# Kernel tuning notes

Hardware: AMD Instinct MI355X
Metric: run time of the kernel (lower is better)

Reference implementation:

```python
import jax, jax.numpy as jnp
import numpy as np

# Dimensions: B jets, P max particles, C coords, F features, K neighbors,
# H hidden units, O MLP output dim. Edge feature dim E = 2*(C+F).
B, P, C, F, K, H, O = 256, 128, 2, 7, 16, 128, 256
E = 2 * (C + F)
BIG = 1e9  # distance assigned to invalid (padded) neighbors


def setup_inputs() -> dict:
    key = jax.random.key(0)
    k1, k2, k3, k4 = jax.random.split(key, 4)
    raw = jax.random.normal(k1, (B, P, C + F), dtype=jnp.float32)
    # per-jet particle counts in [K+2, P]; padding is contiguous at the end
    lengths = jax.random.randint(k2, (B,), K + 2, P + 1)
    mask = (jnp.arange(P)[None, :] < lengths[:, None]).astype(jnp.float32)  # [B,P]
    # zero out padded rows and append mask as the last column (as the layer expects)
    x = jnp.concatenate([raw * mask[..., None], mask[..., None]], axis=-1)  # [B,P,C+F+1]
    W1 = jax.random.normal(k3, (E, H), dtype=jnp.float32) * (1.0 / np.sqrt(E))
    b1 = jnp.zeros((H,), dtype=jnp.float32)
    W2 = jax.random.normal(k4, (H, O), dtype=jnp.float32) * (1.0 / np.sqrt(H))
    b2 = jnp.zeros((O,), dtype=jnp.float32)
    return {"x": x, "W1": W1, "b1": b1, "W2": W2, "b2": b2}


def reference(x, W1, b1, W2, b2):
    coords = x[..., :C]          # [B,P,C]
    feats = x[..., C:-1]         # [B,P,F]
    mask = x[..., -1]            # [B,P] 1=real particle, 0=padding
    valid = mask > 0

    # --- kNN on coordinates (masked, vectorized over jets) ---
    diff = coords[:, :, None, :] - coords[:, None, :, :]      # [B,P,P,C]
    # squared distance: same ordering as tf.norm, avoids sqrt-at-zero issues
    dist2 = jnp.sum(diff * diff, axis=-1)                      # [B,P,P]
    dist2 = jnp.where(valid[:, None, :], dist2, BIG)           # mask padded neighbors
    _, idx = jax.lax.top_k(-dist2, K + 1)                      # [B,P,K+1]
    idx = idx[..., 1:]                                         # drop self -> [B,P,K]

    # --- gather neighbor coords/features ---
    idx_flat = idx.reshape(B, P * K)
    nbr_c = jnp.take_along_axis(coords, idx_flat[..., None], axis=1).reshape(B, P, K, C)
    nbr_f = jnp.take_along_axis(feats, idx_flat[..., None], axis=1).reshape(B, P, K, F)
    ctr_c = jnp.broadcast_to(coords[:, :, None, :], (B, P, K, C))
    ctr_f = jnp.broadcast_to(feats[:, :, None, :], (B, P, K, F))

    # edge features: [coord_i, feat_i, coord_j - coord_i, feat_j - feat_i]
    edge = jnp.concatenate([ctr_c, ctr_f, nbr_c - ctr_c, nbr_f - ctr_f], axis=-1)  # [B,P,K,E]

    # --- MLP + mean aggregation over neighbors ---
    h = jax.nn.relu(edge @ W1 + b1)   # [B,P,K,H]
    h = jax.nn.relu(h @ W2 + b2)      # [B,P,K,O]
    avg = jnp.mean(h, axis=2)         # [B,P,O]

    # append mask column; zero out padded particles (matches _fix_number_of_particles)
    out = jnp.concatenate([avg, jnp.ones((B, P, 1), avg.dtype)], axis=-1) * mask[..., None]
    return out
```

## Files before the change

kernel.cpp:

```cpp
#include <hip/hip_runtime.h>

#define BB 256
#define PP 128
#define KK 16
#define HH 128
#define OO 256
#define EE 18
#define XCH 10
#define BIGD 1000000000.0f
#define GPT 4

typedef __bf16 bf16x8 __attribute__((ext_vector_type(8)));
typedef __bf16 bf16x4 __attribute__((ext_vector_type(4)));
typedef float  f32x4  __attribute__((ext_vector_type(4)));

__global__ __launch_bounds__(256) void pack_w_kernel(const float* __restrict__ W1,
                                                     const float* __restrict__ W2,
                                                     __bf16* __restrict__ W2p,
                                                     __bf16* __restrict__ W1p) {
    const int t = blockIdx.x * 256 + threadIdx.x;
    if (t < 32768) {
        const int j  = t & 7;
        const int l  = (t >> 3) & 63;
        const int ks = (t >> 9) & 3;
        const int ct = t >> 11;
        const int row = ks * 32 + ((l >> 4) * 8) + j;
        const int col = ct * 16 + (l & 15);
        W2p[t] = (__bf16)W2[row * OO + col];
    } else {
        const int t2 = t - 32768;
        const int j  = t2 & 7;
        const int l  = (t2 >> 3) & 63;
        const int nt = t2 >> 9;
        const int k  = ((l >> 4) * 8) + j;
        const int n  = nt * 16 + (l & 15);
        W1p[t2] = (k < EE) ? (__bf16)W1[k * HH + n] : (__bf16)0.0f;
    }
}

__global__ __launch_bounds__(256, 4) void mlp_kernel(const float* __restrict__ x,
                                                     const __bf16* __restrict__ W1p,
                                                     const float* __restrict__ b1,
                                                     const __bf16* __restrict__ W2p,
                                                     const float* __restrict__ b2,
                                                     float* __restrict__ out) {
    __shared__ __bf16 sh1A[16 * 64 * 8];
    __shared__ float  sb1[HH];
    __shared__ float  sb2[OO];
    __shared__ float  smask[GPT];
    __shared__ int    sknn[GPT][KK];

    const int tid = threadIdx.x;
    const int lane = tid & 63;
    const int w = tid >> 6;
    const int quad = lane >> 4;
    const int lcol = lane & 15;

    const int pbase = blockIdx.x * GPT;
    const int bidx = pbase >> 7;
    const int i0 = pbase & (PP - 1);
    const float* xb = x + (size_t)bidx * PP * XCH;
    float* outrow = out + (size_t)pbase * (OO + 1);

    if (tid < HH) sb1[tid] = b1[tid];
    sb2[tid] = b2[tid];
    if (tid < GPT) smask[tid] = xb[(i0 + tid) * XCH + (XCH - 1)];
    __syncthreads();

    const bool allmasked =
        (smask[0] == 0.0f) & (smask[1] == 0.0f) & (smask[2] == 0.0f) & (smask[3] == 0.0f);
    if (allmasked) {
        for (int o = tid; o < GPT * (OO + 1); o += 256) outrow[o] = 0.0f;
        return;
    }

    const int i = i0 + w;
    if (smask[w] != 0.0f) {
        const float cix = xb[i * XCH + 0];
        const float ciy = xb[i * XCH + 1];

        const int j0 = lane, j1 = lane + 64;
        float d0, d1;
        {
            const float2 c0 = *(const float2*)(xb + j0 * XCH);
            const float m0 = xb[j0 * XCH + (XCH - 1)];
            float dx = cix - c0.x, dy = ciy - c0.y;
            d0 = __fadd_rn(__fmul_rn(dx, dx), __fmul_rn(dy, dy));
            if (m0 <= 0.0f || j0 == i) d0 = BIGD;
        }
        {
            const float2 c1 = *(const float2*)(xb + j1 * XCH);
            const float m1 = xb[j1 * XCH + (XCH - 1)];
            float dx = cix - c1.x, dy = ciy - c1.y;
            d1 = __fadd_rn(__fmul_rn(dx, dx), __fmul_rn(dy, dy));
            if (m1 <= 0.0f || j1 == i) d1 = BIGD;
        }

        const unsigned d0b = __float_as_uint(d0);
        const unsigned d1b = __float_as_uint(d1);

        unsigned long long A0 = ~0ull, A1 = ~0ull, W0 = 0ull, W1 = 0ull;
        int need = KK;
        int asz = 2 * 64;

        auto step = [&](unsigned long long q0, unsigned long long q1) {
            const unsigned long long z0 = A0 & q0;
            const unsigned long long z1 = A1 & q1;
            const int c = __popcll(z0) + __popcll(z1);
            if (c == need) { W0 |= z0; W1 |= z1; A0 = A1 = 0ull; need = 0; }
            else if (c > need) { A0 = z0; A1 = z1; asz = c; }
            else { W0 |= z0; W1 |= z1; need -= c; A0 &= ~z0; A1 &= ~z1; asz -= c; }
        };

#pragma unroll 1
        for (int t = 14; t >= 0; --t) {
            const unsigned dg0 = (d0b >> (2 * t + 1)) & 3u;
            const unsigned dg1 = (d1b >> (2 * t + 1)) & 3u;
            const unsigned long long p0_0  = __ballot(dg0 == 0u);
            const unsigned long long p1_0  = __ballot(dg1 == 0u);
            const unsigned long long p0_01 = __ballot(dg0 <= 1u);
            const unsigned long long p1_01 = __ballot(dg1 <= 1u);
            const unsigned long long p0_02 = __ballot(dg0 <= 2u);
            const unsigned long long p1_02 = __ballot(dg1 <= 2u);
            const unsigned long long z0_0  = A0 & p0_0,  z1_0  = A1 & p1_0;
            const unsigned long long z0_01 = A0 & p0_01, z1_01 = A1 & p1_01;
            const unsigned long long z0_02 = A0 & p0_02, z1_02 = A1 & p1_02;
            const int c0  = __popcll(z0_0)  + __popcll(z1_0);
            const int c01 = __popcll(z0_01) + __popcll(z1_01);
            const int c02 = __popcll(z0_02) + __popcll(z1_02);
            if (c0 >= need) {
                A0 = z0_0; A1 = z1_0; asz = c0;
            } else if (c01 >= need) {
                W0 |= z0_0; W1 |= z1_0; need -= c0;
                A0 = z0_01 & ~p0_0; A1 = z1_01 & ~p1_0; asz = c01 - c0;
            } else if (c02 >= need) {
                W0 |= z0_01; W1 |= z1_01; need -= c01;
                A0 = z0_02 & ~p0_01; A1 = z1_02 & ~p1_01; asz = c02 - c01;
            } else {
                W0 |= z0_02; W1 |= z1_02; need -= c02;
                A0 &= ~p0_02; A1 &= ~p1_02; asz -= c02;
            }
            if (asz == need) { W0 |= A0; W1 |= A1; A0 = A1 = 0ull; need = 0; break; }
        }
        if (need) {
            const unsigned long long q0 = __ballot((d0b & 1u) == 0u);
            const unsigned long long q1 = __ballot((d1b & 1u) == 0u);
            step(q0, q1);
        }
        if (need) step(~0ull, 0ull);
        {
            const unsigned long long M5 = 0x00000000FFFFFFFFull;
            const unsigned long long M4 = 0x0000FFFF0000FFFFull;
            const unsigned long long M3 = 0x00FF00FF00FF00FFull;
            const unsigned long long M2 = 0x0F0F0F0F0F0F0F0Full;
            const unsigned long long M1 = 0x3333333333333333ull;
            const unsigned long long M0 = 0x5555555555555555ull;
            if (need) step(M5, M5);
            if (need) step(M4, M4);
            if (need) step(M3, M3);
            if (need) step(M2, M2);
            if (need) step(M1, M1);
            if (need) step(M0, M0);
        }
        W0 |= A0; W1 |= A1;

        unsigned int mb0 = __builtin_amdgcn_mbcnt_lo((unsigned)(W0 & 0xffffffffull), 0u);
        mb0 = __builtin_amdgcn_mbcnt_hi((unsigned)(W0 >> 32), mb0);
        unsigned int mb1 = __builtin_amdgcn_mbcnt_lo((unsigned)(W1 & 0xffffffffull), 0u);
        mb1 = __builtin_amdgcn_mbcnt_hi((unsigned)(W1 >> 32), mb1);
        const int base1 = __popcll(W0);

        if ((W0 >> lane) & 1ull) sknn[w][mb0] = j0;
        if ((W1 >> lane) & 1ull) sknn[w][base1 + mb1] = j1;
    } else {
        if (lane < KK) sknn[w][lane] = 0;
    }

    const int jn = sknn[w][lcol];
    const float* ci = xb + i * XCH;
    const float* cj = xb + jn * XCH;
    const float2 a01 = *(const float2*)(ci + 0);
    const float2 a23 = *(const float2*)(ci + 2);
    const float2 a45 = *(const float2*)(ci + 4);
    const float2 a67 = *(const float2*)(ci + 6);
    const float  a8  = ci[8];
    const float2 n01 = *(const float2*)(cj + 0);
    const float2 n23 = *(const float2*)(cj + 2);
    const float2 n45 = *(const float2*)(cj + 4);
    const float2 n67 = *(const float2*)(cj + 6);
    const float  n8  = cj[8];

    float v[8];
#pragma unroll
    for (int e = 0; e < 8; ++e) v[e] = 0.0f;
    if (quad == 0) {
        v[0] = a01.x; v[1] = a01.y; v[2] = a23.x; v[3] = a23.y;
        v[4] = a45.x; v[5] = a45.y; v[6] = a67.x; v[7] = a67.y;
    } else if (quad == 1) {
        v[0] = a8;
        v[1] = n01.x - a01.x; v[2] = n01.y - a01.y;
        v[3] = n23.x - a23.x; v[4] = n23.y - a23.y;
        v[5] = n45.x - a45.x; v[6] = n45.y - a45.y;
        v[7] = n67.x - a67.x;
    } else if (quad == 2) {
        v[0] = n67.y - a67.y;
        v[1] = n8 - a8;
    }

    bf16x8 ef;
#pragma unroll
    for (int e = 0; e < 8; ++e) ef[e] = (__bf16)v[e];

    bf16x8 wf[8];
#pragma unroll
    for (int nt = 0; nt < 8; ++nt)
        wf[nt] = *(const bf16x8*)&W1p[(size_t)((nt * 64 + lane) * 8)];

    const f32x4 z4 = {0.0f, 0.0f, 0.0f, 0.0f};
    f32x4 h[8];
#pragma unroll
    for (int nt = 0; nt < 8; ++nt)
        h[nt] = __builtin_amdgcn_mfma_f32_16x16x32_bf16(wf[nt], ef, z4, 0, 0, 0);

#pragma unroll
    for (int nt = 0; nt < 8; ++nt) {
        const int ks = nt >> 1;
        const int lp = (((nt * 2 + (quad >> 1)) & 3) << 4) | lcol;
        bf16x4 hv;
#pragma unroll
        for (int r = 0; r < 4; ++r) {
            const int m = nt * 16 + quad * 4 + r;
            hv[r] = (__bf16)fmaxf(h[nt][r] + sb1[m], 0.0f);
        }
        *(bf16x4*)&sh1A[((ks * GPT + w) * 64 + lp) * 8 + (quad & 1) * 4] = hv;
    }
    __syncthreads();

    f32x4 acc[GPT][4];
#pragma unroll
    for (int g = 0; g < GPT; ++g)
#pragma unroll
        for (int ct = 0; ct < 4; ++ct) acc[g][ct] = z4;

#pragma unroll
    for (int ks = 0; ks < 4; ++ks) {
        bf16x8 af[GPT], bfr[4];
#pragma unroll
        for (int g = 0; g < GPT; ++g)
            af[g] = *(const bf16x8*)&sh1A[((ks * GPT + g) * 64 + lane) * 8];
#pragma unroll
        for (int ct = 0; ct < 4; ++ct)
            bfr[ct] = *(const bf16x8*)&W2p[(size_t)((((w * 4 + ct) * 4 + ks) * 64 + lane) * 8)];
#pragma unroll
        for (int g = 0; g < GPT; ++g)
#pragma unroll
            for (int ct = 0; ct < 4; ++ct)
                acc[g][ct] = __builtin_amdgcn_mfma_f32_16x16x32_bf16(
                    af[g], bfr[ct], acc[g][ct], 0, 0, 0);
    }

    float val[4];
#pragma unroll
    for (int g = 0; g < GPT; ++g) {
#pragma unroll
        for (int ct = 0; ct < 4; ++ct) {
            const int col = w * 64 + ct * 16 + lcol;
            const float bc = sb2[col];
            float s = 0.0f;
#pragma unroll
            for (int r = 0; r < 4; ++r) s += fmaxf(acc[g][ct][r] + bc, 0.0f);
            s += __shfl_xor(s, 16, 64);
            s += __shfl_xor(s, 32, 64);
            if (quad == g) val[ct] = s;
        }
    }
    const float m = smask[quad] * (1.0f / KK);
#pragma unroll
    for (int ct = 0; ct < 4; ++ct)
        outrow[(size_t)quad * (OO + 1) + w * 64 + ct * 16 + lcol] = val[ct] * m;
    if (tid < GPT) outrow[(size_t)tid * (OO + 1) + OO] = smask[tid];
}

extern "C" void kernel_launch(void* const* d_in, const int* in_sizes, int n_in,
                              void* d_out, int out_size, void* d_ws, size_t ws_size,
                              hipStream_t stream) {
    const float* x  = (const float*)d_in[0];
    const float* W1 = (const float*)d_in[1];
    const float* b1 = (const float*)d_in[2];
    const float* W2 = (const float*)d_in[3];
    const float* b2 = (const float*)d_in[4];
    float* out = (float*)d_out;

    __bf16* W2p = (__bf16*)d_ws;
    __bf16* W1p = (__bf16*)((char*)d_ws + 65536);

    pack_w_kernel<<<144, 256, 0, stream>>>(W1, W2, W2p, W1p);

    const int nblocks = (BB * PP) / GPT;
    mlp_kernel<<<nblocks, 256, 0, stream>>>(x, W1p, b1, W2p, b2, out);
}
```

Measured before the change: 128.7 us.

## Convert MLP kernel to persistent grid-stride loop over particle chunks

The kernel now launches a fixed grid of 2048 blocks. Each block loops over several 4-particle chunks instead of launching one block per chunk, so the per-block bias loading and launch overhead are paid once per block rather than once per chunk. The mask values are read into registers directly rather than staged through shared memory. An extra barrier per iteration is added to protect the shared h1 buffer from being overwritten before the previous chunk's readers finish. This costs some latency hiding, because fewer independent blocks are in flight.

```diff
diff --git a/kernel.cpp b/kernel.cpp
--- a/kernel.cpp
+++ b/kernel.cpp
@@ -9,6 +9,7 @@
 #define XCH 10
 #define BIGD 1000000000.0f
 #define GPT 4
+#define NBLK 2048
 
 typedef __bf16 bf16x8 __attribute__((ext_vector_type(8)));
 typedef __bf16 bf16x4 __attribute__((ext_vector_type(4)));
@@ -47,7 +48,6 @@
     __shared__ __bf16 sh1A[16 * 64 * 8];
     __shared__ float  sb1[HH];
     __shared__ float  sb2[OO];
-    __shared__ float  smask[GPT];
     __shared__ int    sknn[GPT][KK];
 
     const int tid = threadIdx.x;
@@ -56,229 +56,241 @@
     const int quad = lane >> 4;
     const int lcol = lane & 15;
 
-    const int pbase = blockIdx.x * GPT;
-    const int bidx = pbase >> 7;
-    const int i0 = pbase & (PP - 1);
-    const float* xb = x + (size_t)bidx * PP * XCH;
-    float* outrow = out + (size_t)pbase * (OO + 1);
-
     if (tid < HH) sb1[tid] = b1[tid];
     sb2[tid] = b2[tid];
-    if (tid < GPT) smask[tid] = xb[(i0 + tid) * XCH + (XCH - 1)];
     __syncthreads();
 
-    const bool allmasked =
-        (smask[0] == 0.0f) & (smask[1] == 0.0f) & (smask[2] == 0.0f) & (smask[3] == 0.0f);
-    if (allmasked) {
-        for (int o = tid; o < GPT * (OO + 1); o += 256) outrow[o] = 0.0f;
-        return;
+    const f32x4 z4 = {0.0f, 0.0f, 0.0f, 0.0f};
+
+#pragma unroll 1
+    for (int chunk = blockIdx.x; chunk < (BB * PP) / GPT; chunk += NBLK) {
+        const int pbase = chunk * GPT;
+        const int bidx = pbase >> 7;
+        const int i0 = pbase & (PP - 1);
+        const float* xb = x + (size_t)bidx * PP * XCH;
+        float* outrow = out + (size_t)pbase * (OO + 1);
+
+        const float m0 = xb[(i0 + 0) * XCH + 9];
+        const float m1 = xb[(i0 + 1) * XCH + 9];
+        const float m2 = xb[(i0 + 2) * XCH + 9];
+        const float m3 = xb[(i0 + 3) * XCH + 9];
+        if (m0 == 0.0f && m1 == 0.0f && m2 == 0.0f && m3 == 0.0f) {
+            for (int o = tid; o < GPT * (OO + 1); o += 256) outrow[o] = 0.0f;
+            continue;
+        }
+
+        const int i = i0 + w;
+        const float mw = (w == 0) ? m0 : (w == 1) ? m1 : (w == 2) ? m2 : m3;
+        if (mw != 0.0f) {
+            const float cix = xb[i * XCH + 0];
+            const float ciy = xb[i * XCH + 1];
+
+            const int j0 = lane, j1 = lane + 64;
+            float d0, d1;
+            {
+                const float2 c0 = *(const float2*)(xb + j0 * XCH);
+                const float mj = xb[j0 * XCH + (XCH - 1)];
+                float dx = cix - c0.x, dy = ciy - c0.y;
+                d0 = __fadd_rn(__fmul_rn(dx, dx), __fmul_rn(dy, dy));
+                if (mj <= 0.0f || j0 == i) d0 = BIGD;
+            }
+            {
+                const float2 c1 = *(const float2*)(xb + j1 * XCH);
+                const float mj = xb[j1 * XCH + (XCH - 1)];
+                float dx = cix - c1.x, dy = ciy - c1.y;
+                d1 = __fadd_rn(__fmul_rn(dx, dx), __fmul_rn(dy, dy));
+                if (mj <= 0.0f || j1 == i) d1 = BIGD;
+            }
+
+            const unsigned d0b = __float_as_uint(d0);
+            const unsigned d1b = __float_as_uint(d1);
+
+            unsigned long long A0 = ~0ull, A1 = ~0ull, W0 = 0ull, W1 = 0ull;
+            int need = KK;
+            int asz = 2 * 64;
+
+            auto step = [&](unsigned long long q0, unsigned long long q1) {
+                const unsigned long long z0 = A0 & q0;
+                const unsigned long long z1 = A1 & q1;
+                const int c = __popcll(z0) + __popcll(z1);
+                if (c == need) { W0 |= z0; W1 |= z1; A0 = A1 = 0ull; need = 0; }
+                else if (c > need) { A0 = z0; A1 = z1; asz = c; }
+                else { W0 |= z0; W1 |= z1; need -= c; A0 &= ~z0; A1 &= ~z1; asz -= c; }
+            };
+
+#pragma unroll 1
+            for (int t = 14; t >= 0; --t) {
+                const unsigned dg0 = (d0b >> (2 * t + 1)) & 3u;
+                const unsigned dg1 = (d1b >> (2 * t + 1)) & 3u;
+                const unsigned long long p0_0  = __ballot(dg0 == 0u);
+                const unsigned long long p1_0  = __ballot(dg1 == 0u);
+                const unsigned long long p0_01 = __ballot(dg0 <= 1u);
+                const unsigned long long p1_01 = __ballot(dg1 <= 1u);
+                const unsigned long long p0_02 = __ballot(dg0 <= 2u);
+                const unsigned long long p1_02 = __ballot(dg1 <= 2u);
+                const unsigned long long z0_0  = A0 & p0_0,  z1_0  = A1 & p1_0;
+                const unsigned long long z0_01 = A0 & p0_01, z1_01 = A1 & p1_01;
+                const unsigned long long z0_02 = A0 & p0_02, z1_02 = A1 & p1_02;
+                const int c0  = __popcll(z0_0)  + __popcll(z1_0);
+                const int c01 = __popcll(z0_01) + __popcll(z1_01);
+                const int c02 = __popcll(z0_02) + __popcll(z1_02);
+                if (c0 >= need) {
+                    A0 = z0_0; A1 = z1_0; asz = c0;
+                } else if (c01 >= need) {
+                    W0 |= z0_0; W1 |= z1_0; need -= c0;
+                    A0 = z0_01 & ~p0_0; A1 = z1_01 & ~p1_0; asz = c01 - c0;
+                } else if (c02 >= need) {
+                    W0 |= z0_01; W1 |= z1_01; need -= c01;
+                    A0 = z0_02 & ~p0_01; A1 = z1_02 & ~p1_01; asz = c02 - c01;
+                } else {
+                    W0 |= z0_02; W1 |= z1_02; need -= c02;
+                    A0 &= ~p0_02; A1 &= ~p1_02; asz -= c02;
+                }
+                if (asz == need) { W0 |= A0; W1 |= A1; A0 = A1 = 0ull; need = 0; break; }
+            }
+            if (need) {
+                const unsigned long long q0 = __ballot((d0b & 1u) == 0u);
+                const unsigned long long q1 = __ballot((d1b & 1u) == 0u);
+                step(q0, q1);
+            }
+            if (need) step(~0ull, 0ull);
+            {
+                const unsigned long long M5 = 0x00000000FFFFFFFFull;
+                const unsigned long long M4 = 0x0000FFFF0000FFFFull;
+                const unsigned long long M3 = 0x00FF00FF00FF00FFull;
+                const unsigned long long M2 = 0x0F0F0F0F0F0F0F0Full;
+                const unsigned long long M1 = 0x3333333333333333ull;
+                const unsigned long long M0 = 0x5555555555555555ull;
+                if (need) step(M5, M5);
+                if (need) step(M4, M4);
+                if (need) step(M3, M3);
+                if (need) step(M2, M2);
+                if (need) step(M1, M1);
+                if (need) step(M0, M0);
+            }
+            W0 |= A0; W1 |= A1;
+
+            unsigned int mb0 = __builtin_amdgcn_mbcnt_lo((unsigned)(W0 & 0xffffffffull), 0u);
+            mb0 = __builtin_amdgcn_mbcnt_hi((unsigned)(W0 >> 32), mb0);
+            unsigned int mb1 = __builtin_amdgcn_mbcnt_lo((unsigned)(W1 & 0xffffffffull), 0u);
+            mb1 = __builtin_amdgcn_mbcnt_hi((unsigned)(W1 >> 32), mb1);
+            const int base1 = __popcll(W0);
+
+            if ((W0 >> lane) & 1ull) sknn[w][mb0] = j0;
+            if ((W1 >> lane) & 1ull) sknn[w][base1 + mb1] = j1;
+        } else {
+            if (lane < KK) sknn[w][lane] = 0;
+        }
+
+        const int jn = sknn[w][lcol];
+        const float* ci = xb + i * XCH;
+        const float* cj = xb + jn * XCH;
+        const float2 a01 = *(const float2*)(ci + 0);
+        const float2 a23 = *(const float2*)(ci + 2);
+        const float2 a45 = *(const float2*)(ci + 4);
+        const float2 a67 = *(const float2*)(ci + 6);
+        const float  a8  = ci[8];
+        const float2 n01 = *(const float2*)(cj + 0);
+        const float2 n23 = *(const float2*)(cj + 2);
+        const float2 n45 = *(const float2*)(cj + 4);
+        const float2 n67 = *(const float2*)(cj + 6);
+        const float  n8  = cj[8];
+
+        float v[8];
+#pragma unroll
+        for (int e = 0; e < 8; ++e) v[e] = 0.0f;
+        if (quad == 0) {
+            v[0] = a01.x; v[1] = a01.y; v[2] = a23.x; v[3] = a23.y;
+            v[4] = a45.x; v[5] = a45.y; v[6] = a67.x; v[7] = a67.y;
+        } else if (quad == 1) {
+            v[0] = a8;
+            v[1] = n01.x - a01.x; v[2] = n01.y - a01.y;
+            v[3] = n23.x - a23.x; v[4] = n23.y - a23.y;
+            v[5] = n45.x - a45.x; v[6] = n45.y - a45.y;
+            v[7] = n67.x - a67.x;
+        } else if (quad == 2) {
+            v[0] = n67.y - a67.y;
+            v[1] = n8 - a8;
+        }
+
+        bf16x8 ef;
+#pragma unroll
+        for (int e = 0; e < 8; ++e) ef[e] = (__bf16)v[e];
+
+        bf16x8 wf[8];
+#pragma unroll
+        for (int nt = 0; nt < 8; ++nt)
+            wf[nt] = *(const bf16x8*)&W1p[(size_t)((nt * 64 + lane) * 8)];
+
+        f32x4 h[8];
+#pragma unroll
+        for (int nt = 0; nt < 8; ++nt)
+            h[nt] = __builtin_amdgcn_mfma_f32_16x16x32_bf16(wf[nt], ef, z4, 0, 0, 0);
+
+        __syncthreads();
+
+#pragma unroll
+        for (int nt = 0; nt < 8; ++nt) {
+            const int ks = nt >> 1;
+            const int lp = (((nt * 2 + (quad >> 1)) & 3) << 4) | lcol;
+            bf16x4 hv;
+#pragma unroll
+            for (int r = 0; r < 4; ++r) {
+                const int m = nt * 16 + quad * 4 + r;
+                hv[r] = (__bf16)fmaxf(h[nt][r] + sb1[m], 0.0f);
+            }
+            *(bf16x4*)&sh1A[((ks * GPT + w) * 64 + lp) * 8 + (quad & 1) * 4] = hv;
+        }
+        __syncthreads();
+
+        f32x4 acc[GPT][4];
+#pragma unroll
+        for (int g = 0; g < GPT; ++g)
+#pragma unroll
+            for (int ct = 0; ct < 4; ++ct) acc[g][ct] = z4;
+
+#pragma unroll
+        for (int ks = 0; ks < 4; ++ks) {
+            bf16x8 af[GPT], bfr[4];
+#pragma unroll
+            for (int g = 0; g < GPT; ++g)
+                af[g] = *(const bf16x8*)&sh1A[((ks * GPT + g) * 64 + lane) * 8];
+#pragma unroll
+            for (int ct = 0; ct < 4; ++ct)
+                bfr[ct] = *(const bf16x8*)&W2p[(size_t)((((w * 4 + ct) * 4 + ks) * 64 + lane) * 8)];
+#pragma unroll
+            for (int g = 0; g < GPT; ++g)
+#pragma unroll
+                for (int ct = 0; ct < 4; ++ct)
+                    acc[g][ct] = __builtin_amdgcn_mfma_f32_16x16x32_bf16(
+                        af[g], bfr[ct], acc[g][ct], 0, 0, 0);
+        }
+
+        float val[4];
+#pragma unroll
+        for (int g = 0; g < GPT; ++g) {
+#pragma unroll
+            for (int ct = 0; ct < 4; ++ct) {
+                const int col = w * 64 + ct * 16 + lcol;
+                const float bc = sb2[col];
+                float s = 0.0f;
+#pragma unroll
+                for (int r = 0; r < 4; ++r) s += fmaxf(acc[g][ct][r] + bc, 0.0f);
+                s += __shfl_xor(s, 16, 64);
+                s += __shfl_xor(s, 32, 64);
+                if (quad == g) val[ct] = s;
+            }
+        }
+        const float mq = (quad == 0) ? m0 : (quad == 1) ? m1 : (quad == 2) ? m2 : m3;
+        const float msc = mq * (1.0f / KK);
+#pragma unroll
+        for (int ct = 0; ct < 4; ++ct)
+            outrow[(size_t)quad * (OO + 1) + w * 64 + ct * 16 + lcol] = val[ct] * msc;
+        if (tid < GPT) {
+            const float mt = (tid == 0) ? m0 : (tid == 1) ? m1 : (tid == 2) ? m2 : m3;
+            outrow[(size_t)tid * (OO + 1) + OO] = mt;
+        }
     }
-
-    const int i = i0 + w;
-    if (smask[w] != 0.0f) {
-        const float cix = xb[i * XCH + 0];
-        const float ciy = xb[i * XCH + 1];
-
-        const int j0 = lane, j1 = lane + 64;
-        float d0, d1;
-        {
-            const float2 c0 = *(const float2*)(xb + j0 * XCH);
-            const float m0 = xb[j0 * XCH + (XCH - 1)];
-            float dx = cix - c0.x, dy = ciy - c0.y;
-            d0 = __fadd_rn(__fmul_rn(dx, dx), __fmul_rn(dy, dy));
-            if (m0 <= 0.0f || j0 == i) d0 = BIGD;
-        }
-        {
-            const float2 c1 = *(const float2*)(xb + j1 * XCH);
-            const float m1 = xb[j1 * XCH + (XCH - 1)];
-            float dx = cix - c1.x, dy = ciy - c1.y;
-            d1 = __fadd_rn(__fmul_rn(dx, dx), __fmul_rn(dy, dy));
-            if (m1 <= 0.0f || j1 == i) d1 = BIGD;
-        }
-
-        const unsigned d0b = __float_as_uint(d0);
-        const unsigned d1b = __float_as_uint(d1);
-
-        unsigned long long A0 = ~0ull, A1 = ~0ull, W0 = 0ull, W1 = 0ull;
-        int need = KK;
-        int asz = 2 * 64;
-
-        auto step = [&](unsigned long long q0, unsigned long long q1) {
-            const unsigned long long z0 = A0 & q0;
-            const unsigned long long z1 = A1 & q1;
-            const int c = __popcll(z0) + __popcll(z1);
-            if (c == need) { W0 |= z0; W1 |= z1; A0 = A1 = 0ull; need = 0; }
-            else if (c > need) { A0 = z0; A1 = z1; asz = c; }
-            else { W0 |= z0; W1 |= z1; need -= c; A0 &= ~z0; A1 &= ~z1; asz -= c; }
-        };
-
-#pragma unroll 1
-        for (int t = 14; t >= 0; --t) {
-            const unsigned dg0 = (d0b >> (2 * t + 1)) & 3u;
-            const unsigned dg1 = (d1b >> (2 * t + 1)) & 3u;
-            const unsigned long long p0_0  = __ballot(dg0 == 0u);
-            const unsigned long long p1_0  = __ballot(dg1 == 0u);
-            const unsigned long long p0_01 = __ballot(dg0 <= 1u);
-            const unsigned long long p1_01 = __ballot(dg1 <= 1u);
-            const unsigned long long p0_02 = __ballot(dg0 <= 2u);
-            const unsigned long long p1_02 = __ballot(dg1 <= 2u);
-            const unsigned long long z0_0  = A0 & p0_0,  z1_0  = A1 & p1_0;
-            const unsigned long long z0_01 = A0 & p0_01, z1_01 = A1 & p1_01;
-            const unsigned long long z0_02 = A0 & p0_02, z1_02 = A1 & p1_02;
-            const int c0  = __popcll(z0_0)  + __popcll(z1_0);
-            const int c01 = __popcll(z0_01) + __popcll(z1_01);
-            const int c02 = __popcll(z0_02) + __popcll(z1_02);
-            if (c0 >= need) {
-                A0 = z0_0; A1 = z1_0; asz = c0;
-            } else if (c01 >= need) {
-                W0 |= z0_0; W1 |= z1_0; need -= c0;
-                A0 = z0_01 & ~p0_0; A1 = z1_01 & ~p1_0; asz = c01 - c0;
-            } else if (c02 >= need) {
-                W0 |= z0_01; W1 |= z1_01; need -= c01;
-                A0 = z0_02 & ~p0_01; A1 = z1_02 & ~p1_01; asz = c02 - c01;
-            } else {
-                W0 |= z0_02; W1 |= z1_02; need -= c02;
-                A0 &= ~p0_02; A1 &= ~p1_02; asz -= c02;
-            }
-            if (asz == need) { W0 |= A0; W1 |= A1; A0 = A1 = 0ull; need = 0; break; }
-        }
-        if (need) {
-            const unsigned long long q0 = __ballot((d0b & 1u) == 0u);
-            const unsigned long long q1 = __ballot((d1b & 1u) == 0u);
-            step(q0, q1);
-        }
-        if (need) step(~0ull, 0ull);
-        {
-            const unsigned long long M5 = 0x00000000FFFFFFFFull;
-            const unsigned long long M4 = 0x0000FFFF0000FFFFull;
-            const unsigned long long M3 = 0x00FF00FF00FF00FFull;
-            const unsigned long long M2 = 0x0F0F0F0F0F0F0F0Full;
-            const unsigned long long M1 = 0x3333333333333333ull;
-            const unsigned long long M0 = 0x5555555555555555ull;
-            if (need) step(M5, M5);
-            if (need) step(M4, M4);
-            if (need) step(M3, M3);
-            if (need) step(M2, M2);
-            if (need) step(M1, M1);
-            if (need) step(M0, M0);
-        }
-        W0 |= A0; W1 |= A1;
-
-        unsigned int mb0 = __builtin_amdgcn_mbcnt_lo((unsigned)(W0 & 0xffffffffull), 0u);
-        mb0 = __builtin_amdgcn_mbcnt_hi((unsigned)(W0 >> 32), mb0);
-        unsigned int mb1 = __builtin_amdgcn_mbcnt_lo((unsigned)(W1 & 0xffffffffull), 0u);
-        mb1 = __builtin_amdgcn_mbcnt_hi((unsigned)(W1 >> 32), mb1);
-        const int base1 = __popcll(W0);
-
-        if ((W0 >> lane) & 1ull) sknn[w][mb0] = j0;
-        if ((W1 >> lane) & 1ull) sknn[w][base1 + mb1] = j1;
-    } else {
-        if (lane < KK) sknn[w][lane] = 0;
-    }
-
-    const int jn = sknn[w][lcol];
-    const float* ci = xb + i * XCH;
-    const float* cj = xb + jn * XCH;
-    const float2 a01 = *(const float2*)(ci + 0);
-    const float2 a23 = *(const float2*)(ci + 2);
-    const float2 a45 = *(const float2*)(ci + 4);
-    const float2 a67 = *(const float2*)(ci + 6);
-    const float  a8  = ci[8];
-    const float2 n01 = *(const float2*)(cj + 0);
-    const float2 n23 = *(const float2*)(cj + 2);
-    const float2 n45 = *(const float2*)(cj + 4);
-    const float2 n67 = *(const float2*)(cj + 6);
-    const float  n8  = cj[8];
-
-    float v[8];
-#pragma unroll
-    for (int e = 0; e < 8; ++e) v[e] = 0.0f;
-    if (quad == 0) {
-        v[0] = a01.x; v[1] = a01.y; v[2] = a23.x; v[3] = a23.y;
-        v[4] = a45.x; v[5] = a45.y; v[6] = a67.x; v[7] = a67.y;
-    } else if (quad == 1) {
-        v[0] = a8;
-        v[1] = n01.x - a01.x; v[2] = n01.y - a01.y;
-        v[3] = n23.x - a23.x; v[4] = n23.y - a23.y;
-        v[5] = n45.x - a45.x; v[6] = n45.y - a45.y;
-        v[7] = n67.x - a67.x;
-    } else if (quad == 2) {
-        v[0] = n67.y - a67.y;
-        v[1] = n8 - a8;
-    }
-
-    bf16x8 ef;
-#pragma unroll
-    for (int e = 0; e < 8; ++e) ef[e] = (__bf16)v[e];
-
-    bf16x8 wf[8];
-#pragma unroll
-    for (int nt = 0; nt < 8; ++nt)
-        wf[nt] = *(const bf16x8*)&W1p[(size_t)((nt * 64 + lane) * 8)];
-
-    const f32x4 z4 = {0.0f, 0.0f, 0.0f, 0.0f};
-    f32x4 h[8];
-#pragma unroll
-    for (int nt = 0; nt < 8; ++nt)
-        h[nt] = __builtin_amdgcn_mfma_f32_16x16x32_bf16(wf[nt], ef, z4, 0, 0, 0);
-
-#pragma unroll
-    for (int nt = 0; nt < 8; ++nt) {
-        const int ks = nt >> 1;
-        const int lp = (((nt * 2 + (quad >> 1)) & 3) << 4) | lcol;
-        bf16x4 hv;
-#pragma unroll
-        for (int r = 0; r < 4; ++r) {
-            const int m = nt * 16 + quad * 4 + r;
-            hv[r] = (__bf16)fmaxf(h[nt][r] + sb1[m], 0.0f);
-        }
-        *(bf16x4*)&sh1A[((ks * GPT + w) * 64 + lp) * 8 + (quad & 1) * 4] = hv;
-    }
-    __syncthreads();
-
-    f32x4 acc[GPT][4];
-#pragma unroll
-    for (int g = 0; g < GPT; ++g)
-#pragma unroll
-        for (int ct = 0; ct < 4; ++ct) acc[g][ct] = z4;
-
-#pragma unroll
-    for (int ks = 0; ks < 4; ++ks) {
-        bf16x8 af[GPT], bfr[4];
-#pragma unroll
-        for (int g = 0; g < GPT; ++g)
-            af[g] = *(const bf16x8*)&sh1A[((ks * GPT + g) * 64 + lane) * 8];
-#pragma unroll
-        for (int ct = 0; ct < 4; ++ct)
-            bfr[ct] = *(const bf16x8*)&W2p[(size_t)((((w * 4 + ct) * 4 + ks) * 64 + lane) * 8)];
-#pragma unroll
-        for (int g = 0; g < GPT; ++g)
-#pragma unroll
-            for (int ct = 0; ct < 4; ++ct)
-                acc[g][ct] = __builtin_amdgcn_mfma_f32_16x16x32_bf16(
-                    af[g], bfr[ct], acc[g][ct], 0, 0, 0);
-    }
-
-    float val[4];
-#pragma unroll
-    for (int g = 0; g < GPT; ++g) {
-#pragma unroll
-        for (int ct = 0; ct < 4; ++ct) {
-            const int col = w * 64 + ct * 16 + lcol;
-            const float bc = sb2[col];
-            float s = 0.0f;
-#pragma unroll
-            for (int r = 0; r < 4; ++r) s += fmaxf(acc[g][ct][r] + bc, 0.0f);
-            s += __shfl_xor(s, 16, 64);
-            s += __shfl_xor(s, 32, 64);
-            if (quad == g) val[ct] = s;
-        }
-    }
-    const float m = smask[quad] * (1.0f / KK);
-#pragma unroll
-    for (int ct = 0; ct < 4; ++ct)
-        outrow[(size_t)quad * (OO + 1) + w * 64 + ct * 16 + lcol] = val[ct] * m;
-    if (tid < GPT) outrow[(size_t)tid * (OO + 1) + OO] = smask[tid];
 }
 
 extern "C" void kernel_launch(void* const* d_in, const int* in_sizes, int n_in,
@@ -296,6 +308,5 @@
 
     pack_w_kernel<<<144, 256, 0, stream>>>(W1, W2, W2p, W1p);
 
-    const int nblocks = (BB * PP) / GPT;
-    mlp_kernel<<<nblocks, 256, 0, stream>>>(x, W1p, b1, W2p, b2, out);
+    mlp_kernel<<<NBLK, 256, 0, stream>>>(x, W1p, b1, W2p, b2, out);
 }
```

New measurement: 173.0 us. 34.4% more time.
